# Kernel tuning notes

Hardware: AMD Instinct MI355X
Metric: run time of the kernel (lower is better)

## Reference

```python
import jax, jax.numpy as jnp
import numpy as np

B, C, D, H, W = 2, 64, 3, 96, 96
CD = C * D  # conv1x1 channel count = in_dim * 3


def setup_inputs() -> dict:
    key = jax.random.key(0)
    ks = jax.random.split(key, 7)
    s = 1.0 / np.sqrt(CD)
    x = jax.random.normal(ks[0], (B, C, D, H, W), dtype=jnp.float32)
    Wq = jax.random.uniform(ks[1], (CD, CD), jnp.float32, -s, s)
    bq = jax.random.uniform(ks[2], (CD,), jnp.float32, -s, s)
    Wk = jax.random.uniform(ks[3], (CD, CD), jnp.float32, -s, s)
    bk = jax.random.uniform(ks[4], (CD,), jnp.float32, -s, s)
    Wv = jax.random.uniform(ks[5], (CD, CD), jnp.float32, -s, s)
    bv = jax.random.uniform(ks[6], (CD,), jnp.float32, -s, s)
    return {"x": x, "Wq": Wq, "bq": bq, "Wk": Wk, "bk": bk, "Wv": Wv, "bv": bv}


def reference(x, Wq, bq, Wk, bk, Wv, bv):
    b, c, d, h, w = x.shape
    n = h * w
    xr = x.reshape(b, c * d, n)  # [B, CD, N]; conv1x1 == channel matmul
    q = jnp.einsum('oc,bcn->bon', Wq, xr) + bq[:, None]  # [B, CD, N]
    k = jnp.einsum('oc,bcn->bon', Wk, xr) + bk[:, None]
    v = jnp.einsum('oc,bcn->bon', Wv, xr) + bv[:, None]
    energy = jnp.einsum('bcn,bcm->bnm', q, k)            # [B, N, N]
    attention = jax.nn.softmax(energy, axis=-1)
    # out = bmm(value, attention^T): out[b,c,m] = sum_n v[b,c,n] * attn[b,m,n]
    out = jnp.einsum('bcn,bmn->bcm', v, attention)       # [B, CD, N]
    return out.reshape(b, c, d, h, w)
```

## Files before the change

### kernel.cpp

```cpp
#include <hip/hip_runtime.h>

#define NSEQ  9216
#define CDIM  192
#define LOG2E 1.44269504088896f

typedef _Float16 h8_t  __attribute__((ext_vector_type(8)));
typedef _Float16 h4_t  __attribute__((ext_vector_type(4)));
typedef _Float16 h2_t  __attribute__((ext_vector_type(2)));
typedef float    f4_t  __attribute__((ext_vector_type(4)));
typedef float    f16v  __attribute__((ext_vector_type(16)));

static __device__ inline unsigned pack2(float a, float b) {
    union { h2_t h; unsigned u; } x;
    x.h = (h2_t){(_Float16)a, (_Float16)b};
    return x.u;
}

__global__ __launch_bounds__(256) void wconv_kernel(
    const float* __restrict__ Wq, const float* __restrict__ Wk,
    const float* __restrict__ Wv, _Float16* __restrict__ Wh)
{
    int i = blockIdx.x * 256 + threadIdx.x;
    if (i >= 3 * 9216) return;
    const float* src = (i < 9216) ? Wq : (i < 18432 ? Wk : Wv);
    float s = (i < 9216) ? LOG2E : 1.f;
    int r = i % 9216;
    f4_t w = ((const f4_t*)src)[r];
    h4_t h = {(_Float16)(w[0]*s), (_Float16)(w[1]*s),
              (_Float16)(w[2]*s), (_Float16)(w[3]*s)};
    ((h4_t*)Wh)[i] = h;
}

__global__ __launch_bounds__(256) void proj_kernel(
    const float* __restrict__ x, const _Float16* __restrict__ Wh,
    const float* __restrict__ bq, const float* __restrict__ bk,
    const float* __restrict__ bv,
    _Float16* __restrict__ QT, _Float16* __restrict__ KT, _Float16* __restrict__ Vg)
{
    const int tid  = threadIdx.x;
    const int lane = tid & 63, wave = tid >> 6;
    const int L31  = lane & 31, hi = lane >> 5;
    const int idx  = blockIdx.x * 4 + wave;
    const int mat  = idx / 576;
    const int rem  = idx % 576;
    const int b    = rem / 288;
    const int n0   = (rem % 288) * 32;
    const int n    = n0 + L31;

    h8_t bf[12];
    #pragma unroll
    for (int t = 0; t < 12; t++) {
        h8_t h;
        #pragma unroll
        for (int j = 0; j < 8; j++)
            h[j] = (_Float16)x[(size_t)(b * CDIM + t * 16 + hi * 8 + j) * NSEQ + n];
        bf[t] = h;
    }

    const _Float16* W = Wh + mat * CDIM * CDIM;
    const float* bias = (mat == 0) ? bq : (mat == 1 ? bk : bv);
    const float bscale = (mat == 0) ? LOG2E : 1.f;

    f16v acc[6];
    #pragma unroll
    for (int s = 0; s < 6; s++)
        #pragma unroll
        for (int r = 0; r < 16; r++) acc[s][r] = 0.f;

    #pragma unroll
    for (int t = 0; t < 12; t++) {
        #pragma unroll
        for (int s = 0; s < 6; s++) {
            h8_t a = *(const h8_t*)(W + (s * 32 + L31) * CDIM + t * 16 + hi * 8);
            acc[s] = __builtin_amdgcn_mfma_f32_32x32x16_f16(a, bf[t], acc[s], 0, 0, 0);
        }
    }

    if (mat < 2) {
        _Float16* dst = ((mat == 0) ? QT : KT) + ((size_t)b * NSEQ + n) * CDIM;
        #pragma unroll
        for (int s = 0; s < 6; s++) {
            #pragma unroll
            for (int g = 0; g < 4; g++) {
                f4_t bb = *(const f4_t*)&bias[s * 32 + 8 * g + 4 * hi];
                h4_t h = {(_Float16)(acc[s][4*g+0] + bb[0] * bscale),
                          (_Float16)(acc[s][4*g+1] + bb[1] * bscale),
                          (_Float16)(acc[s][4*g+2] + bb[2] * bscale),
                          (_Float16)(acc[s][4*g+3] + bb[3] * bscale)};
                *(h4_t*)(dst + s * 32 + 8 * g + 4 * hi) = h;
            }
        }
    } else {
        #pragma unroll
        for (int s = 0; s < 6; s++) {
            #pragma unroll
            for (int g = 0; g < 4; g++) {
                f4_t bb = *(const f4_t*)&bias[s * 32 + 8 * g + 4 * hi];
                #pragma unroll
                for (int r = 0; r < 4; r++) {
                    int o = s * 32 + 8 * g + 4 * hi + r;
                    Vg[((size_t)b * CDIM + o) * NSEQ + n] =
                        (_Float16)(acc[s][4*g+r] + bb[r]);
                }
            }
        }
    }
}

template<int NSPLIT>
__global__ __launch_bounds__(256, 2) void flash_kernel(
    const _Float16* __restrict__ QT, const _Float16* __restrict__ KTg,
    const _Float16* __restrict__ Vg,
    _Float16* __restrict__ O_part, float* __restrict__ m_part, float* __restrict__ l_part)
{
    constexpr int KPS    = NSEQ / NSPLIT;
    constexpr int KITERS = KPS / 32;
    constexpr int KBUF   = 32 * 200;
    __shared__ __align__(16) _Float16 Sh[25600];

    const int tid  = threadIdx.x;
    const int lane = tid & 63, wave = tid >> 6;
    const int L31  = lane & 31, hi = lane >> 5;
    const int qtile = blockIdx.x, split = blockIdx.y, b = blockIdx.z;
    const int q0 = qtile * 128 + wave * 32;

    h8_t qf[12];
    const _Float16* qbase = QT + ((size_t)b * NSEQ + q0 + L31) * CDIM + hi * 8;
    #pragma unroll
    for (int t = 0; t < 12; t++) qf[t] = *(const h8_t*)(qbase + t * 16);

    f16v acc[6];
    #pragma unroll
    for (int s = 0; s < 6; s++)
        #pragma unroll
        for (int r = 0; r < 16; r++) acc[s][r] = 0.f;
    float m_run = -__builtin_inff();
    float l_run = 0.f;

    const _Float16* ksrc = KTg + ((size_t)b * NSEQ + split * KPS) * CDIM;
    const _Float16* vsrc = Vg + (size_t)b * CDIM * NSEQ + split * KPS;

    int kds[3], vds[3];
    const _Float16 *kgl[3], *vgl[3];
    #pragma unroll
    for (int r = 0; r < 3; r++) {
        int i = r * 256 + tid;
        kds[r] = (i / 24) * 200 + (i % 24) * 8;
        kgl[r] = ksrc + i * 8;
        int c = i >> 2, seg = i & 3;
        vds[r] = KBUF + c * 40 + seg * 8;
        vgl[r] = vsrc + (size_t)c * NSEQ + seg * 8;
    }

    h8_t kreg[3], vreg[3];
    #pragma unroll
    for (int r = 0; r < 3; r++) kreg[r] = *(const h8_t*)(kgl[r]);
    #pragma unroll
    for (int r = 0; r < 3; r++) vreg[r] = *(const h8_t*)(vgl[r]);

    for (int kt = 0; kt < KITERS; kt++) {
        __syncthreads();
        #pragma unroll
        for (int r = 0; r < 3; r++) *(h8_t*)(Sh + kds[r]) = kreg[r];
        #pragma unroll
        for (int r = 0; r < 3; r++) *(h8_t*)(Sh + vds[r]) = vreg[r];
        __syncthreads();
        if (kt + 1 < KITERS) {
            #pragma unroll
            for (int r = 0; r < 3; r++)
                kreg[r] = *(const h8_t*)(kgl[r] + (kt + 1) * 32 * CDIM);
            #pragma unroll
            for (int r = 0; r < 3; r++)
                vreg[r] = *(const h8_t*)(vgl[r] + (kt + 1) * 32);
        }

        f16v st;
        #pragma unroll
        for (int r = 0; r < 16; r++) st[r] = 0.f;
        #pragma unroll
        for (int t = 0; t < 12; t++) {
            h8_t a = *(const h8_t*)(Sh + L31 * 200 + t * 16 + hi * 8);
            st = __builtin_amdgcn_mfma_f32_32x32x16_f16(a, qf[t], st, 0, 0, 0);
        }

        float mx = st[0];
        #pragma unroll
        for (int r = 1; r < 16; r++) mx = fmaxf(mx, st[r]);
        mx = fmaxf(mx, __shfl_xor(mx, 32));
        float m_new = fmaxf(m_run, mx);

        float p[16], psum = 0.f;
        #pragma unroll
        for (int r = 0; r < 16; r++) {
            p[r] = __builtin_exp2f(st[r] - m_new);
            psum += p[r];
        }

        if (__any(m_new > m_run)) {
            float alpha = __builtin_exp2f(m_run - m_new);
            l_run = l_run * alpha + psum;
            #pragma unroll
            for (int cs = 0; cs < 6; cs++)
                #pragma unroll
                for (int r = 0; r < 16; r++) acc[cs][r] *= alpha;
        } else {
            l_run += psum;
        }
        m_run = m_new;

        unsigned pk[8];
        #pragma unroll
        for (int t2 = 0; t2 < 4; t2++) {
            pk[2*t2]   = pack2(p[4*t2+0], p[4*t2+1]);
            pk[2*t2+1] = pack2(p[4*t2+2], p[4*t2+3]);
        }
        unsigned recv0 = __shfl_xor(hi ? pk[0] : pk[2], 32);
        unsigned recv1 = __shfl_xor(hi ? pk[1] : pk[3], 32);
        unsigned recv2 = __shfl_xor(hi ? pk[4] : pk[6], 32);
        unsigned recv3 = __shfl_xor(hi ? pk[5] : pk[7], 32);

        union { h8_t h; unsigned u[4]; } pb0, pb1;
        pb0.u[0] = hi ? recv0 : pk[0];
        pb0.u[1] = hi ? recv1 : pk[1];
        pb0.u[2] = hi ? pk[2] : recv0;
        pb0.u[3] = hi ? pk[3] : recv1;
        pb1.u[0] = hi ? recv2 : pk[4];
        pb1.u[1] = hi ? recv3 : pk[5];
        pb1.u[2] = hi ? pk[6] : recv2;
        pb1.u[3] = hi ? pk[7] : recv3;

        #pragma unroll
        for (int ks = 0; ks < 2; ks++) {
            h8_t pb = ks ? pb1.h : pb0.h;
            #pragma unroll
            for (int cs = 0; cs < 6; cs++) {
                h8_t va = *(const h8_t*)(Sh + KBUF + (cs * 32 + L31) * 40 + ks * 16 + hi * 8);
                acc[cs] = __builtin_amdgcn_mfma_f32_32x32x16_f16(va, pb, acc[cs], 0, 0, 0);
            }
        }
    }

    float l_tot = l_run + __shfl_xor(l_run, 32);
    const size_t pw = (size_t)(b * NSPLIT + split) * NSEQ + q0;
    if (lane < 32) {
        m_part[pw + lane] = m_run;
        l_part[pw + lane] = l_tot;
    }
    __syncthreads();
    _Float16* T = Sh + wave * 6400;
    #pragma unroll
    for (int cs = 0; cs < 6; cs++)
        #pragma unroll
        for (int g = 0; g < 4; g++) {
            h4_t hh = {(_Float16)acc[cs][4*g+0], (_Float16)acc[cs][4*g+1],
                       (_Float16)acc[cs][4*g+2], (_Float16)acc[cs][4*g+3]};
            *(h4_t*)(T + L31 * 200 + cs * 32 + 8 * g + 4 * hi) = hh;
        }
    _Float16* ob = O_part + pw * CDIM;
    #pragma unroll
    for (int it = 0; it < 12; it++) {
        int i = it * 64 + lane;
        int qq = i / 24, col = i % 24;
        h8_t h = *(const h8_t*)(T + qq * 200 + col * 8);
        *(h8_t*)(ob + (size_t)qq * CDIM + col * 8) = h;
    }
}

template<int NS>
__global__ __launch_bounds__(256) void combine_kernel(
    const _Float16* __restrict__ O_part, const float* __restrict__ m_part,
    const float* __restrict__ l_part, float* __restrict__ out)
{
    __shared__ float Cs[CDIM][33];
    __shared__ float winv[NS][32];
    const int tid = threadIdx.x;
    const int b  = blockIdx.y;
    const int n0 = blockIdx.x * 32;

    if (tid < 32) {
        int n = n0 + tid;
        float mm[NS], ll[NS], ms = -__builtin_inff();
        #pragma unroll
        for (int s = 0; s < NS; s++) {
            mm[s] = m_part[(b * NS + s) * NSEQ + n];
            ll[s] = l_part[(b * NS + s) * NSEQ + n];
            ms = fmaxf(ms, mm[s]);
        }
        float denom = 0.f;
        #pragma unroll
        for (int s = 0; s < NS; s++) {
            float w = __builtin_exp2f(mm[s] - ms);
            mm[s] = w;
            denom += w * ll[s];
        }
        #pragma unroll
        for (int s = 0; s < NS; s++) winv[s][tid] = mm[s] / denom;
    }
    __syncthreads();

    for (int i = tid; i < 32 * 96; i += 256) {
        int nl = i / 96, cp = i % 96;
        float v0 = 0.f, v1 = 0.f;
        #pragma unroll
        for (int s = 0; s < NS; s++) {
            h2_t op = *(const h2_t*)(O_part +
                ((size_t)(b * NS + s) * NSEQ + n0 + nl) * CDIM + cp * 2);
            float w = winv[s][nl];
            v0 += w * (float)op[0];
            v1 += w * (float)op[1];
        }
        Cs[cp * 2][nl] = v0;
        Cs[cp * 2 + 1][nl] = v1;
    }
    __syncthreads();
    for (int i = tid; i < CDIM * 32; i += 256) {
        int nl = i & 31, c = i >> 5;
        out[((size_t)b * CDIM + c) * NSEQ + n0 + nl] = Cs[c][nl];
    }
}

extern "C" void kernel_launch(void* const* d_in, const int* in_sizes, int n_in,
                              void* d_out, int out_size, void* d_ws, size_t ws_size,
                              hipStream_t stream)
{
    const float* x  = (const float*)d_in[0];
    const float* Wq = (const float*)d_in[1];
    const float* bq = (const float*)d_in[2];
    const float* Wk = (const float*)d_in[3];
    const float* bk = (const float*)d_in[4];
    const float* Wv = (const float*)d_in[5];
    const float* bv = (const float*)d_in[6];
    float* out = (float*)d_out;

    char* ws = (char*)d_ws;
    _Float16* QT = (_Float16*)(ws);
    _Float16* KT = (_Float16*)(ws + 7077888);
    _Float16* Vg = (_Float16*)(ws + 14155776);
    char* tail = ws + 21233664;
    _Float16* Wh = (_Float16*)tail;
    _Float16* O_part = (_Float16*)tail;

    wconv_kernel<<<108, 256, 0, stream>>>(Wq, Wk, Wv, Wh);
    proj_kernel<<<432, 256, 0, stream>>>(x, Wh, bq, bk, bv, QT, KT, Vg);

    const size_t need8 = 21233664ull + 8 * 7077888ull + 2 * 589824ull;
    const size_t need4 = 21233664ull + 4 * 7077888ull + 2 * 294912ull;
    if (ws_size >= need8) {
        float* m_part = (float*)(tail + 8 * 7077888ull);
        float* l_part = (float*)(tail + 8 * 7077888ull + 589824ull);
        flash_kernel<8><<<dim3(72, 8, 2), 256, 0, stream>>>(QT, KT, Vg, O_part, m_part, l_part);
        combine_kernel<8><<<dim3(288, 2), 256, 0, stream>>>(O_part, m_part, l_part, out);
    } else if (ws_size >= need4) {
        float* m_part = (float*)(tail + 4 * 7077888ull);
        float* l_part = (float*)(tail + 4 * 7077888ull + 294912ull);
        flash_kernel<4><<<dim3(72, 4, 2), 256, 0, stream>>>(QT, KT, Vg, O_part, m_part, l_part);
        combine_kernel<4><<<dim3(288, 2), 256, 0, stream>>>(O_part, m_part, l_part, out);
    } else {
        float* m_part = (float*)(tail + 2 * 7077888ull);
        float* l_part = (float*)(tail + 2 * 7077888ull + 147456ull);
        flash_kernel<2><<<dim3(72, 2, 2), 256, 0, stream>>>(QT, KT, Vg, O_part, m_part, l_part);
        combine_kernel<2><<<dim3(288, 2), 256, 0, stream>>>(O_part, m_part, l_part, out);
    }
}
```

Before: 301.0 us.

## Double flash key tile to 64, fuse QKV projections per block, widen combine tile

```diff
diff --git a/kernel.cpp b/kernel.cpp
--- a/kernel.cpp
+++ b/kernel.cpp
@@ -31,7 +31,7 @@
     ((h4_t*)Wh)[i] = h;
 }
 
-__global__ __launch_bounds__(256) void proj_kernel(
+__global__ __launch_bounds__(128) void proj_kernel(
     const float* __restrict__ x, const _Float16* __restrict__ Wh,
     const float* __restrict__ bq, const float* __restrict__ bk,
     const float* __restrict__ bv,
@@ -40,11 +40,9 @@
     const int tid  = threadIdx.x;
     const int lane = tid & 63, wave = tid >> 6;
     const int L31  = lane & 31, hi = lane >> 5;
-    const int idx  = blockIdx.x * 4 + wave;
-    const int mat  = idx / 576;
-    const int rem  = idx % 576;
-    const int b    = rem / 288;
-    const int n0   = (rem % 288) * 32;
+    const int idx  = blockIdx.x * 2 + wave;
+    const int b    = idx / 288;
+    const int n0   = (idx % 288) * 32;
     const int n    = n0 + L31;
 
     h8_t bf[12];
@@ -57,50 +55,53 @@
         bf[t] = h;
     }
 
-    const _Float16* W = Wh + mat * CDIM * CDIM;
-    const float* bias = (mat == 0) ? bq : (mat == 1 ? bk : bv);
-    const float bscale = (mat == 0) ? LOG2E : 1.f;
-
-    f16v acc[6];
-    #pragma unroll
-    for (int s = 0; s < 6; s++)
-        #pragma unroll
-        for (int r = 0; r < 16; r++) acc[s][r] = 0.f;
-
-    #pragma unroll
-    for (int t = 0; t < 12; t++) {
-        #pragma unroll
-        for (int s = 0; s < 6; s++) {
-            h8_t a = *(const h8_t*)(W + (s * 32 + L31) * CDIM + t * 16 + hi * 8);
-            acc[s] = __builtin_amdgcn_mfma_f32_32x32x16_f16(a, bf[t], acc[s], 0, 0, 0);
-        }
-    }
-
-    if (mat < 2) {
-        _Float16* dst = ((mat == 0) ? QT : KT) + ((size_t)b * NSEQ + n) * CDIM;
-        #pragma unroll
-        for (int s = 0; s < 6; s++) {
-            #pragma unroll
-            for (int g = 0; g < 4; g++) {
-                f4_t bb = *(const f4_t*)&bias[s * 32 + 8 * g + 4 * hi];
-                h4_t h = {(_Float16)(acc[s][4*g+0] + bb[0] * bscale),
-                          (_Float16)(acc[s][4*g+1] + bb[1] * bscale),
-                          (_Float16)(acc[s][4*g+2] + bb[2] * bscale),
-                          (_Float16)(acc[s][4*g+3] + bb[3] * bscale)};
-                *(h4_t*)(dst + s * 32 + 8 * g + 4 * hi) = h;
-            }
-        }
-    } else {
-        #pragma unroll
-        for (int s = 0; s < 6; s++) {
-            #pragma unroll
-            for (int g = 0; g < 4; g++) {
-                f4_t bb = *(const f4_t*)&bias[s * 32 + 8 * g + 4 * hi];
+    const float* biases[3] = {bq, bk, bv};
+    for (int mat = 0; mat < 3; mat++) {
+        const _Float16* W = Wh + mat * CDIM * CDIM;
+        const float* bias = biases[mat];
+        const float bscale = (mat == 0) ? LOG2E : 1.f;
+
+        f16v acc[6];
+        #pragma unroll
+        for (int s = 0; s < 6; s++)
+            #pragma unroll
+            for (int r = 0; r < 16; r++) acc[s][r] = 0.f;
+
+        #pragma unroll
+        for (int t = 0; t < 12; t++) {
+            #pragma unroll
+            for (int s = 0; s < 6; s++) {
+                h8_t a = *(const h8_t*)(W + (s * 32 + L31) * CDIM + t * 16 + hi * 8);
+                acc[s] = __builtin_amdgcn_mfma_f32_32x32x16_f16(a, bf[t], acc[s], 0, 0, 0);
+            }
+        }
+
+        if (mat < 2) {
+            _Float16* dst = ((mat == 0) ? QT : KT) + ((size_t)b * NSEQ + n) * CDIM;
+            #pragma unroll
+            for (int s = 0; s < 6; s++) {
                 #pragma unroll
-                for (int r = 0; r < 4; r++) {
-                    int o = s * 32 + 8 * g + 4 * hi + r;
-                    Vg[((size_t)b * CDIM + o) * NSEQ + n] =
-                        (_Float16)(acc[s][4*g+r] + bb[r]);
+                for (int g = 0; g < 4; g++) {
+                    f4_t bb = *(const f4_t*)&bias[s * 32 + 8 * g + 4 * hi];
+                    h4_t h = {(_Float16)(acc[s][4*g+0] + bb[0] * bscale),
+                              (_Float16)(acc[s][4*g+1] + bb[1] * bscale),
+                              (_Float16)(acc[s][4*g+2] + bb[2] * bscale),
+                              (_Float16)(acc[s][4*g+3] + bb[3] * bscale)};
+                    *(h4_t*)(dst + s * 32 + 8 * g + 4 * hi) = h;
+                }
+            }
+        } else {
+            #pragma unroll
+            for (int s = 0; s < 6; s++) {
+                #pragma unroll
+                for (int g = 0; g < 4; g++) {
+                    f4_t bb = *(const f4_t*)&bias[s * 32 + 8 * g + 4 * hi];
+                    #pragma unroll
+                    for (int r = 0; r < 4; r++) {
+                        int o = s * 32 + 8 * g + 4 * hi + r;
+                        Vg[((size_t)b * CDIM + o) * NSEQ + n] =
+                            (_Float16)(acc[s][4*g+r] + bb[r]);
+                    }
                 }
             }
         }
@@ -114,9 +115,9 @@
     _Float16* __restrict__ O_part, float* __restrict__ m_part, float* __restrict__ l_part)
 {
     constexpr int KPS    = NSEQ / NSPLIT;
-    constexpr int KITERS = KPS / 32;
-    constexpr int KBUF   = 32 * 200;
-    __shared__ __align__(16) _Float16 Sh[25600];
+    constexpr int KITERS = KPS / 64;
+    constexpr int KBUF   = 64 * 200;
+    __shared__ __align__(16) _Float16 Sh[38912];
 
     const int tid  = threadIdx.x;
     const int lane = tid & 63, wave = tid >> 6;
@@ -140,60 +141,73 @@
     const _Float16* ksrc = KTg + ((size_t)b * NSEQ + split * KPS) * CDIM;
     const _Float16* vsrc = Vg + (size_t)b * CDIM * NSEQ + split * KPS;
 
-    int kds[3], vds[3];
-    const _Float16 *kgl[3], *vgl[3];
-    #pragma unroll
-    for (int r = 0; r < 3; r++) {
+    int kds[6], vds[6];
+    const _Float16 *kgl[6], *vgl[6];
+    #pragma unroll
+    for (int r = 0; r < 6; r++) {
         int i = r * 256 + tid;
         kds[r] = (i / 24) * 200 + (i % 24) * 8;
         kgl[r] = ksrc + i * 8;
-        int c = i >> 2, seg = i & 3;
-        vds[r] = KBUF + c * 40 + seg * 8;
+        int c = i >> 3, seg = i & 7;
+        vds[r] = KBUF + c * 136 + seg * 8;
         vgl[r] = vsrc + (size_t)c * NSEQ + seg * 8;
     }
 
-    h8_t kreg[3], vreg[3];
-    #pragma unroll
-    for (int r = 0; r < 3; r++) kreg[r] = *(const h8_t*)(kgl[r]);
-    #pragma unroll
-    for (int r = 0; r < 3; r++) vreg[r] = *(const h8_t*)(vgl[r]);
+    h8_t kreg[6], vreg[6];
+    #pragma unroll
+    for (int r = 0; r < 6; r++) kreg[r] = *(const h8_t*)(kgl[r]);
+    #pragma unroll
+    for (int r = 0; r < 6; r++) vreg[r] = *(const h8_t*)(vgl[r]);
 
     for (int kt = 0; kt < KITERS; kt++) {
         __syncthreads();
         #pragma unroll
-        for (int r = 0; r < 3; r++) *(h8_t*)(Sh + kds[r]) = kreg[r];
-        #pragma unroll
-        for (int r = 0; r < 3; r++) *(h8_t*)(Sh + vds[r]) = vreg[r];
+        for (int r = 0; r < 6; r++) *(h8_t*)(Sh + kds[r]) = kreg[r];
+        #pragma unroll
+        for (int r = 0; r < 6; r++) *(h8_t*)(Sh + vds[r]) = vreg[r];
         __syncthreads();
         if (kt + 1 < KITERS) {
             #pragma unroll
-            for (int r = 0; r < 3; r++)
-                kreg[r] = *(const h8_t*)(kgl[r] + (kt + 1) * 32 * CDIM);
-            #pragma unroll
-            for (int r = 0; r < 3; r++)
-                vreg[r] = *(const h8_t*)(vgl[r] + (kt + 1) * 32);
-        }
-
-        f16v st;
-        #pragma unroll
-        for (int r = 0; r < 16; r++) st[r] = 0.f;
+            for (int r = 0; r < 6; r++)
+                kreg[r] = *(const h8_t*)(kgl[r] + (kt + 1) * 64 * CDIM);
+            #pragma unroll
+            for (int r = 0; r < 6; r++)
+                vreg[r] = *(const h8_t*)(vgl[r] + (kt + 1) * 64);
+        }
+
+        f16v st[2];
+        #pragma unroll
+        for (int s = 0; s < 2; s++)
+            #pragma unroll
+            for (int r = 0; r < 16; r++) st[s][r] = 0.f;
         #pragma unroll
         for (int t = 0; t < 12; t++) {
-            h8_t a = *(const h8_t*)(Sh + L31 * 200 + t * 16 + hi * 8);
-            st = __builtin_amdgcn_mfma_f32_32x32x16_f16(a, qf[t], st, 0, 0, 0);
-        }
-
-        float mx = st[0];
-        #pragma unroll
-        for (int r = 1; r < 16; r++) mx = fmaxf(mx, st[r]);
+            h8_t a0 = *(const h8_t*)(Sh + L31 * 200 + t * 16 + hi * 8);
+            st[0] = __builtin_amdgcn_mfma_f32_32x32x16_f16(a0, qf[t], st[0], 0, 0, 0);
+            h8_t a1 = *(const h8_t*)(Sh + (32 + L31) * 200 + t * 16 + hi * 8);
+            st[1] = __builtin_amdgcn_mfma_f32_32x32x16_f16(a1, qf[t], st[1], 0, 0, 0);
+        }
+
+        float mx = fmaxf(st[0][0], st[1][0]);
+        #pragma unroll
+        for (int r = 1; r < 16; r++) mx = fmaxf(mx, fmaxf(st[0][r], st[1][r]));
         mx = fmaxf(mx, __shfl_xor(mx, 32));
         float m_new = fmaxf(m_run, mx);
 
-        float p[16], psum = 0.f;
-        #pragma unroll
-        for (int r = 0; r < 16; r++) {
-            p[r] = __builtin_exp2f(st[r] - m_new);
-            psum += p[r];
+        unsigned pk[16];
+        float psum = 0.f;
+        #pragma unroll
+        for (int s = 0; s < 2; s++) {
+            #pragma unroll
+            for (int g = 0; g < 4; g++) {
+                float e0 = __builtin_exp2f(st[s][4*g+0] - m_new);
+                float e1 = __builtin_exp2f(st[s][4*g+1] - m_new);
+                float e2 = __builtin_exp2f(st[s][4*g+2] - m_new);
+                float e3 = __builtin_exp2f(st[s][4*g+3] - m_new);
+                psum += (e0 + e1) + (e2 + e3);
+                pk[8*s + 2*g]     = pack2(e0, e1);
+                pk[8*s + 2*g + 1] = pack2(e2, e3);
+            }
         }
 
         if (__any(m_new > m_run)) {
@@ -208,34 +222,22 @@
         }
         m_run = m_new;
 
-        unsigned pk[8];
-        #pragma unroll
-        for (int t2 = 0; t2 < 4; t2++) {
-            pk[2*t2]   = pack2(p[4*t2+0], p[4*t2+1]);
-            pk[2*t2+1] = pack2(p[4*t2+2], p[4*t2+3]);
-        }
-        unsigned recv0 = __shfl_xor(hi ? pk[0] : pk[2], 32);
-        unsigned recv1 = __shfl_xor(hi ? pk[1] : pk[3], 32);
-        unsigned recv2 = __shfl_xor(hi ? pk[4] : pk[6], 32);
-        unsigned recv3 = __shfl_xor(hi ? pk[5] : pk[7], 32);
-
-        union { h8_t h; unsigned u[4]; } pb0, pb1;
-        pb0.u[0] = hi ? recv0 : pk[0];
-        pb0.u[1] = hi ? recv1 : pk[1];
-        pb0.u[2] = hi ? pk[2] : recv0;
-        pb0.u[3] = hi ? pk[3] : recv1;
-        pb1.u[0] = hi ? recv2 : pk[4];
-        pb1.u[1] = hi ? recv3 : pk[5];
-        pb1.u[2] = hi ? pk[6] : recv2;
-        pb1.u[3] = hi ? pk[7] : recv3;
-
-        #pragma unroll
-        for (int ks = 0; ks < 2; ks++) {
-            h8_t pb = ks ? pb1.h : pb0.h;
+        #pragma unroll
+        for (int ks = 0; ks < 4; ks++) {
+            unsigned send0 = hi ? pk[4*ks]     : pk[4*ks + 2];
+            unsigned send1 = hi ? pk[4*ks + 1] : pk[4*ks + 3];
+            unsigned recv0 = __shfl_xor(send0, 32);
+            unsigned recv1 = __shfl_xor(send1, 32);
+            union { h8_t h; unsigned u[4]; } pb;
+            pb.u[0] = hi ? recv0         : pk[4*ks];
+            pb.u[1] = hi ? recv1         : pk[4*ks + 1];
+            pb.u[2] = hi ? pk[4*ks + 2]  : recv0;
+            pb.u[3] = hi ? pk[4*ks + 3]  : recv1;
             #pragma unroll
             for (int cs = 0; cs < 6; cs++) {
-                h8_t va = *(const h8_t*)(Sh + KBUF + (cs * 32 + L31) * 40 + ks * 16 + hi * 8);
-                acc[cs] = __builtin_amdgcn_mfma_f32_32x32x16_f16(va, pb, acc[cs], 0, 0, 0);
+                h8_t va = *(const h8_t*)(Sh + KBUF + (cs * 32 + L31) * 136
+                                         + ks * 16 + hi * 8);
+                acc[cs] = __builtin_amdgcn_mfma_f32_32x32x16_f16(va, pb.h, acc[cs], 0, 0, 0);
             }
         }
     }
@@ -271,13 +273,13 @@
     const _Float16* __restrict__ O_part, const float* __restrict__ m_part,
     const float* __restrict__ l_part, float* __restrict__ out)
 {
-    __shared__ float Cs[CDIM][33];
-    __shared__ float winv[NS][32];
+    __shared__ float Cs[CDIM][65];
+    __shared__ float winv[NS][64];
     const int tid = threadIdx.x;
     const int b  = blockIdx.y;
-    const int n0 = blockIdx.x * 32;
-
-    if (tid < 32) {
+    const int n0 = blockIdx.x * 64;
+
+    if (tid < 64) {
         int n = n0 + tid;
         float mm[NS], ll[NS], ms = -__builtin_inff();
         #pragma unroll
@@ -298,7 +300,7 @@
     }
     __syncthreads();
 
-    for (int i = tid; i < 32 * 96; i += 256) {
+    for (int i = tid; i < 64 * 96; i += 256) {
         int nl = i / 96, cp = i % 96;
         float v0 = 0.f, v1 = 0.f;
         #pragma unroll
@@ -313,8 +315,8 @@
         Cs[cp * 2 + 1][nl] = v1;
     }
     __syncthreads();
-    for (int i = tid; i < CDIM * 32; i += 256) {
-        int nl = i & 31, c = i >> 5;
+    for (int i = tid; i < CDIM * 64; i += 256) {
+        int nl = i & 63, c = i >> 6;
         out[((size_t)b * CDIM + c) * NSEQ + n0 + nl] = Cs[c][nl];
     }
 }
@@ -341,7 +343,7 @@
     _Float16* O_part = (_Float16*)tail;
 
     wconv_kernel<<<108, 256, 0, stream>>>(Wq, Wk, Wv, Wh);
-    proj_kernel<<<432, 256, 0, stream>>>(x, Wh, bq, bk, bv, QT, KT, Vg);
+    proj_kernel<<<288, 128, 0, stream>>>(x, Wh, bq, bk, bv, QT, KT, Vg);
 
     const size_t need8 = 21233664ull + 8 * 7077888ull + 2 * 589824ull;
     const size_t need4 = 21233664ull + 4 * 7077888ull + 2 * 294912ull;
@@ -349,16 +351,16 @@
         float* m_part = (float*)(tail + 8 * 7077888ull);
         float* l_part = (float*)(tail + 8 * 7077888ull + 589824ull);
         flash_kernel<8><<<dim3(72, 8, 2), 256, 0, stream>>>(QT, KT, Vg, O_part, m_part, l_part);
-        combine_kernel<8><<<dim3(288, 2), 256, 0, stream>>>(O_part, m_part, l_part, out);
+        combine_kernel<8><<<dim3(144, 2), 256, 0, stream>>>(O_part, m_part, l_part, out);
     } else if (ws_size >= need4) {
         float* m_part = (float*)(tail + 4 * 7077888ull);
         float* l_part = (float*)(tail + 4 * 7077888ull + 294912ull);
         flash_kernel<4><<<dim3(72, 4, 2), 256, 0, stream>>>(QT, KT, Vg, O_part, m_part, l_part);
-        combine_kernel<4><<<dim3(288, 2), 256, 0, stream>>>(O_part, m_part, l_part, out);
+        combine_kernel<4><<<dim3(144, 2), 256, 0, stream>>>(O_part, m_part, l_part, out);
     } else {
         float* m_part = (float*)(tail + 2 * 7077888ull);
         float* l_part = (float*)(tail + 2 * 7077888ull + 147456ull);
         flash_kernel<2><<<dim3(72, 2, 2), 256, 0, stream>>>(QT, KT, Vg, O_part, m_part, l_part);
-        combine_kernel<2><<<dim3(288, 2), 256, 0, stream>>>(O_part, m_part, l_part, out);
-    }
-}
+        combine_kernel<2><<<dim3(144, 2), 256, 0, stream>>>(O_part, m_part, l_part, out);
+    }
+}
```

Measured after the change: 343.1 us. +14.0%, slower.
